# Optimization experiments

Measured on AMD Instinct MI355X. Metric: run time of the kernel, lower is better.

The kernel has to match this reference:

```python
import jax, jax.numpy as jnp
import numpy as np

B, IN_SIZE, P = 16384, 4096, 8
D = IN_SIZE // P  # 512


def setup_inputs() -> dict:
    key = jax.random.key(0)
    ks = jax.random.split(key, 10)
    bound = 1.0 / np.sqrt(D)  # fan_in = int_dim
    return {
        "x": jax.random.normal(ks[0], (B, IN_SIZE), dtype=jnp.float32),
        "weights1": jax.random.uniform(ks[1], (P, D, D), jnp.float32, -bound, bound),
        "bias1": jax.random.uniform(ks[2], (IN_SIZE,), jnp.float32, -bound, bound),
        "weights2": jax.random.uniform(ks[3], (P, D, D), jnp.float32, -bound, bound),
        "bias2": jax.random.uniform(ks[4], (IN_SIZE,), jnp.float32, -bound, bound),
        # trainable swish params (init 0 as in torch code)
        "gamma1": jnp.zeros((IN_SIZE,), jnp.float32),
        "beta1": jnp.zeros((IN_SIZE,), jnp.float32),
        "gamma3": jnp.zeros((IN_SIZE,), jnp.float32),
        "beta3": jnp.zeros((IN_SIZE,), jnp.float32),
        # Affine norms (scalar gain/bias)
        "gain1": jnp.ones((1,), jnp.float32),
        "nbias1": jnp.zeros((1,), jnp.float32),
        "gain3": jnp.ones((1,), jnp.float32),
        "nbias3": jnp.zeros((1,), jnp.float32),
    }


def _swish(x, gamma, beta):
    # f(x) = (gamma + sigmoid(beta*x) * (1-gamma)) * x
    return (gamma + jax.nn.sigmoid(beta * x) * (1.0 - gamma)) * x


def _block_matmul(x, w):
    # x: [B, IN_SIZE] -> [B, P, D]; block-diagonal matmul == batched per-partition GEMM
    xb = x.reshape(x.shape[0], P, D)
    return jnp.einsum("bpd,pde->bpe", xb, w).reshape(x.shape[0], IN_SIZE)


def reference(x, weights1, bias1, weights2, bias2, gamma1, beta1, gamma3, beta3,
              gain1, nbias1, gain3, nbias3):
    o1 = _swish(_block_matmul(x * gain1 + nbias1, weights1) + bias1, gamma1, beta1)
    o2 = _swish(_block_matmul(o1 * gain3 + nbias3, weights2) + bias2, gamma3, beta3) + x
    return o2
```

## Files before the change

kernel.cpp:

```cpp
#include <hip/hip_runtime.h>
#include <cstdint>
#include <cstddef>


#define B_ROWS 16384
#define IN_SZ  4096
#define P_PART 8
#define D_DIM  512

typedef unsigned short ushort_t;
typedef __attribute__((ext_vector_type(8))) short short8;
typedef __attribute__((ext_vector_type(4))) float f32x4;

__device__ inline unsigned short f2bf(float f) {
  union { float f; unsigned int u; } c; c.f = f;
  unsigned int u = c.u;
  return (unsigned short)((u + 0x7fffu + ((u >> 16) & 1u)) >> 16);
}

__device__ inline void gld_to_lds16(const void* g, void* l) {
  __builtin_amdgcn_global_load_lds((const __attribute__((address_space(1))) void*)g,
                                   (__attribute__((address_space(3))) void*)l,
                                   16, 0, 0);
}

__global__ __launch_bounds__(256) void wconv_kernel(const float* __restrict__ w1,
                                                    const float* __restrict__ w2,
                                                    ushort_t* __restrict__ wt1,
                                                    ushort_t* __restrict__ wt2) {
  __shared__ float tile[64][68];
  const int p = blockIdx.z & 7;
  const float*  src = (blockIdx.z < 8) ? w1 : w2;
  ushort_t*     dst = (blockIdx.z < 8) ? wt1 : wt2;
  const int k0 = blockIdx.x * 64;
  const int n0 = blockIdx.y * 64;
  const int t = threadIdx.x;

  const float* base = src + ((size_t)p * D_DIM + k0) * D_DIM + n0;
#pragma unroll
  for (int i = 0; i < 4; ++i) {
    int f = t + i * 256;
    int kr = f >> 4;
    int c4 = f & 15;
    float4 v = *(const float4*)(base + (size_t)kr * D_DIM + c4 * 4);
    *(float4*)(&tile[kr][c4 * 4]) = v;
  }
  __syncthreads();
  ushort_t* obase = dst + ((size_t)p * D_DIM + n0) * D_DIM + k0;
#pragma unroll
  for (int i = 0; i < 4; ++i) {
    int f = t + i * 256;
    int nr = f >> 4;
    int kc = (f & 15) * 4;
    unsigned int lo = f2bf(tile[kc + 0][nr]) | ((unsigned int)f2bf(tile[kc + 1][nr]) << 16);
    unsigned int hi = f2bf(tile[kc + 2][nr]) | ((unsigned int)f2bf(tile[kc + 3][nr]) << 16);
    uint2 pk; pk.x = lo; pk.y = hi;
    *(uint2*)(obase + (size_t)nr * D_DIM + kc) = pk;
  }
}

__global__ __launch_bounds__(256) void gemm1_kernel(
    const float* __restrict__ x, const ushort_t* __restrict__ wt1,
    const float* __restrict__ bias1, const float* __restrict__ gamma1,
    const float* __restrict__ beta1,
    const float* __restrict__ gain1, const float* __restrict__ nbias1,
    const float* __restrict__ gain3, const float* __restrict__ nbias3,
    ushort_t* __restrict__ o1) {
  __shared__ __align__(16) ushort_t As[128 * 64];
  __shared__ __align__(16) ushort_t Bs[128 * 64];

  const int t = threadIdx.x;
  const int lane = t & 63, wid = t >> 6;
  const int wm = wid & 1, wn = wid >> 1;
  const int l15 = lane & 15, quad = lane >> 4;
  const int m0 = blockIdx.x * 128;
  const int n0 = blockIdx.y * 128;
  const int p  = blockIdx.z;

  const float g1 = gain1[0], nb1 = nbias1[0];
  const float g3 = gain3[0], nb3 = nbias3[0];

  f32x4 acc[4][4];
#pragma unroll
  for (int i = 0; i < 4; ++i)
#pragma unroll
    for (int j = 0; j < 4; ++j) acc[i][j] = (f32x4)(0.0f);

  const ushort_t* wbase = wt1 + (size_t)p * D_DIM * D_DIM;

  for (int kt = 0; kt < 8; ++kt) {
    __syncthreads();
    const float* xtile = x + (size_t)m0 * IN_SZ + p * D_DIM + kt * 64;
#pragma unroll
    for (int i = 0; i < 8; ++i) {
      int f = t + i * 256;
      int row = f >> 4, c4 = f & 15;
      float4 v = *(const float4*)(xtile + (size_t)row * IN_SZ + c4 * 4);
      v.x = v.x * g1 + nb1; v.y = v.y * g1 + nb1;
      v.z = v.z * g1 + nb1; v.w = v.w * g1 + nb1;
      uint2 pk;
      pk.x = f2bf(v.x) | ((unsigned int)f2bf(v.y) << 16);
      pk.y = f2bf(v.z) | ((unsigned int)f2bf(v.w) << 16);
      *(uint2*)(&As[f * 4]) = pk;
    }
#pragma unroll
    for (int c = 0; c < 4; ++c) {
      int off = (wid * 4 + c) * 1024;
      int lb = off + lane * 16;
      int n = lb >> 7, kb = lb & 127;
      const ushort_t* g = wbase + (size_t)(n0 + n) * D_DIM + kt * 64 + (kb >> 1);
      gld_to_lds16(g, (char*)Bs + off);
    }
    __syncthreads();
#pragma unroll
    for (int kk = 0; kk < 2; ++kk) {
      const int kof = kk * 32 + quad * 8;
      short8 a[4], b[4];
#pragma unroll
      for (int i = 0; i < 4; ++i)
        a[i] = *(const short8*)(&As[(wm * 64 + i * 16 + l15) * 64 + kof]);
#pragma unroll
      for (int j = 0; j < 4; ++j)
        b[j] = *(const short8*)(&Bs[(wn * 64 + j * 16 + l15) * 64 + kof]);
#pragma unroll
      for (int i = 0; i < 4; ++i)
#pragma unroll
        for (int j = 0; j < 4; ++j)
          acc[i][j] = __builtin_amdgcn_mfma_f32_16x16x32_bf16(a[i], b[j], acc[i][j], 0, 0, 0);
    }
  }

  const int colg0 = p * D_DIM + n0 + wn * 64;
  const int row0 = m0 + wm * 64 + quad * 4;
#pragma unroll
  for (int j = 0; j < 4; ++j) {
    int col = colg0 + j * 16 + l15;
    float bv = bias1[col], ga = gamma1[col], be = beta1[col];
#pragma unroll
    for (int i = 0; i < 4; ++i) {
      int r0 = row0 + i * 16;
#pragma unroll
      for (int r = 0; r < 4; ++r) {
        float v = acc[i][j][r] + bv;
        float sg = 1.0f / (1.0f + __expf(-be * v));
        float o = (ga + sg * (1.0f - ga)) * v;
        o = o * g3 + nb3;
        o1[(size_t)(r0 + r) * IN_SZ + col] = f2bf(o);
      }
    }
  }
}

__global__ __launch_bounds__(256) void gemm2_kernel(
    const ushort_t* __restrict__ o1, const ushort_t* __restrict__ wt2,
    const float* __restrict__ bias2, const float* __restrict__ gamma3,
    const float* __restrict__ beta3,
    const float* __restrict__ x, float* __restrict__ out) {
  __shared__ __align__(16) ushort_t As[128 * 64];
  __shared__ __align__(16) ushort_t Bs[128 * 64];

  const int t = threadIdx.x;
  const int lane = t & 63, wid = t >> 6;
  const int wm = wid & 1, wn = wid >> 1;
  const int l15 = lane & 15, quad = lane >> 4;
  const int m0 = blockIdx.x * 128;
  const int n0 = blockIdx.y * 128;
  const int p  = blockIdx.z;

  f32x4 acc[4][4];
#pragma unroll
  for (int i = 0; i < 4; ++i)
#pragma unroll
    for (int j = 0; j < 4; ++j) acc[i][j] = (f32x4)(0.0f);

  const ushort_t* wbase = wt2 + (size_t)p * D_DIM * D_DIM;

  for (int kt = 0; kt < 8; ++kt) {
    __syncthreads();
#pragma unroll
    for (int c = 0; c < 4; ++c) {
      int off = (wid * 4 + c) * 1024;
      int lb = off + lane * 16;
      int m = lb >> 7, kb = lb & 127;
      const ushort_t* g = o1 + (size_t)(m0 + m) * IN_SZ + p * D_DIM + kt * 64 + (kb >> 1);
      gld_to_lds16(g, (char*)As + off);
    }
#pragma unroll
    for (int c = 0; c < 4; ++c) {
      int off = (wid * 4 + c) * 1024;
      int lb = off + lane * 16;
      int n = lb >> 7, kb = lb & 127;
      const ushort_t* g = wbase + (size_t)(n0 + n) * D_DIM + kt * 64 + (kb >> 1);
      gld_to_lds16(g, (char*)Bs + off);
    }
    __syncthreads();
#pragma unroll
    for (int kk = 0; kk < 2; ++kk) {
      const int kof = kk * 32 + quad * 8;
      short8 a[4], b[4];
#pragma unroll
      for (int i = 0; i < 4; ++i)
        a[i] = *(const short8*)(&As[(wm * 64 + i * 16 + l15) * 64 + kof]);
#pragma unroll
      for (int j = 0; j < 4; ++j)
        b[j] = *(const short8*)(&Bs[(wn * 64 + j * 16 + l15) * 64 + kof]);
#pragma unroll
      for (int i = 0; i < 4; ++i)
#pragma unroll
        for (int j = 0; j < 4; ++j)
          acc[i][j] = __builtin_amdgcn_mfma_f32_16x16x32_bf16(a[i], b[j], acc[i][j], 0, 0, 0);
    }
  }

  const int colg0 = p * D_DIM + n0 + wn * 64;
  const int row0 = m0 + wm * 64 + quad * 4;
#pragma unroll
  for (int j = 0; j < 4; ++j) {
    int col = colg0 + j * 16 + l15;
    float bv = bias2[col], ga = gamma3[col], be = beta3[col];
#pragma unroll
    for (int i = 0; i < 4; ++i) {
      int r0 = row0 + i * 16;
#pragma unroll
      for (int r = 0; r < 4; ++r) {
        float v = acc[i][j][r] + bv;
        float sg = 1.0f / (1.0f + __expf(-be * v));
        float o = (ga + sg * (1.0f - ga)) * v;
        size_t idx = (size_t)(r0 + r) * IN_SZ + col;
        out[idx] = o + x[idx];
      }
    }
  }
}

extern "C" void kernel_launch(void* const* d_in, const int* in_sizes, int n_in,
                              void* d_out, int out_size, void* d_ws, size_t ws_size,
                              hipStream_t stream) {
  const float* x      = (const float*)d_in[0];
  const float* w1     = (const float*)d_in[1];
  const float* b1     = (const float*)d_in[2];
  const float* w2     = (const float*)d_in[3];
  const float* b2     = (const float*)d_in[4];
  const float* gamma1 = (const float*)d_in[5];
  const float* beta1  = (const float*)d_in[6];
  const float* gamma3 = (const float*)d_in[7];
  const float* beta3  = (const float*)d_in[8];
  const float* gain1  = (const float*)d_in[9];
  const float* nbias1 = (const float*)d_in[10];
  const float* gain3  = (const float*)d_in[11];
  const float* nbias3 = (const float*)d_in[12];
  float* out = (float*)d_out;

  ushort_t* o1  = (ushort_t*)d_ws;
  ushort_t* wt1 = (ushort_t*)((char*)d_ws + (size_t)B_ROWS * IN_SZ * 2);
  ushort_t* wt2 = wt1 + (size_t)P_PART * D_DIM * D_DIM;

  wconv_kernel<<<dim3(8, 8, 16), 256, 0, stream>>>(w1, w2, wt1, wt2);
  gemm1_kernel<<<dim3(128, 4, 8), 256, 0, stream>>>(x, wt1, b1, gamma1, beta1,
                                                    gain1, nbias1, gain3, nbias3, o1);
  gemm2_kernel<<<dim3(128, 4, 8), 256, 0, stream>>>(o1, wt2, b2, gamma3, beta3, x, out);
}
```

Before: 866.6 us.

## Fuse both block GEMMs into one kernel keeping intermediate in swizzled LDS

Replaces the two separate GEMM kernels with one fused kernel. Each block owns a 64-row by 512-column slab of one partition, and the first layer's activation stays in XOR-swizzled shared memory instead of going through a global bf16 buffer. Weight fragments are now read straight from global memory (L2) by each wave instead of being staged in LDS. This removes the global write and re-read of the intermediate and one launch. The cost is 64KB of LDS per block, 128 accumulators per thread (occupancy pressure), and uncoalesced per-lane weight loads from global.

```diff
diff --git a/kernel.cpp b/kernel.cpp
--- a/kernel.cpp
+++ b/kernel.cpp
@@ -18,10 +18,9 @@
   return (unsigned short)((u + 0x7fffu + ((u >> 16) & 1u)) >> 16);
 }
 
-__device__ inline void gld_to_lds16(const void* g, void* l) {
-  __builtin_amdgcn_global_load_lds((const __attribute__((address_space(1))) void*)g,
-                                   (__attribute__((address_space(3))) void*)l,
-                                   16, 0, 0);
+__device__ inline int sw_off(int m, int k) {
+  int c = k >> 3;
+  return (m << 9) | (((c ^ (m & 7)) << 3) | (k & 7));
 }
 
 __global__ __launch_bounds__(256) void wconv_kernel(const float* __restrict__ w1,
@@ -59,174 +58,119 @@
   }
 }
 
-__global__ __launch_bounds__(256) void gemm1_kernel(
-    const float* __restrict__ x, const ushort_t* __restrict__ wt1,
+__device__ inline void gemm_k512(const ushort_t* __restrict__ xs,
+                                 const ushort_t* __restrict__ wp,
+                                 int l15, int quad, f32x4 acc[4][8]) {
+  for (int kk = 0; kk < 16; ++kk) {
+    const int k0 = kk * 32 + quad * 8;
+    short8 a[4];
+#pragma unroll
+    for (int i = 0; i < 4; ++i)
+      a[i] = *(const short8*)(&xs[sw_off(i * 16 + l15, k0)]);
+#pragma unroll
+    for (int jh = 0; jh < 2; ++jh) {
+      short8 b[4];
+#pragma unroll
+      for (int j = 0; j < 4; ++j)
+        b[j] = *(const short8*)(wp + (size_t)(jh * 64 + j * 16 + l15) * D_DIM + k0);
+#pragma unroll
+      for (int i = 0; i < 4; ++i)
+#pragma unroll
+        for (int j = 0; j < 4; ++j)
+          acc[i][jh * 4 + j] =
+              __builtin_amdgcn_mfma_f32_16x16x32_bf16(a[i], b[j], acc[i][jh * 4 + j], 0, 0, 0);
+    }
+  }
+}
+
+__global__ __launch_bounds__(256, 2) void fused_kernel(
+    const float* __restrict__ x,
+    const ushort_t* __restrict__ wt1, const ushort_t* __restrict__ wt2,
     const float* __restrict__ bias1, const float* __restrict__ gamma1,
     const float* __restrict__ beta1,
+    const float* __restrict__ bias2, const float* __restrict__ gamma3,
+    const float* __restrict__ beta3,
     const float* __restrict__ gain1, const float* __restrict__ nbias1,
     const float* __restrict__ gain3, const float* __restrict__ nbias3,
-    ushort_t* __restrict__ o1) {
-  __shared__ __align__(16) ushort_t As[128 * 64];
-  __shared__ __align__(16) ushort_t Bs[128 * 64];
+    float* __restrict__ out) {
+  __shared__ __align__(16) ushort_t xs[64 * 512];
 
   const int t = threadIdx.x;
-  const int lane = t & 63, wid = t >> 6;
-  const int wm = wid & 1, wn = wid >> 1;
+  const int lane = t & 63, w = t >> 6;
   const int l15 = lane & 15, quad = lane >> 4;
-  const int m0 = blockIdx.x * 128;
-  const int n0 = blockIdx.y * 128;
-  const int p  = blockIdx.z;
+  const int p = blockIdx.x;
+  const int m0 = blockIdx.y * 64;
 
   const float g1 = gain1[0], nb1 = nbias1[0];
   const float g3 = gain3[0], nb3 = nbias3[0];
 
-  f32x4 acc[4][4];
+  const float* xg = x + (size_t)m0 * IN_SZ + p * D_DIM;
+#pragma unroll
+  for (int i = 0; i < 32; ++i) {
+    int f = t + i * 256;
+    int row = f >> 7, c4 = f & 127;
+    float4 v = *(const float4*)(xg + (size_t)row * IN_SZ + c4 * 4);
+    v.x = v.x * g1 + nb1; v.y = v.y * g1 + nb1;
+    v.z = v.z * g1 + nb1; v.w = v.w * g1 + nb1;
+    uint2 pk;
+    pk.x = f2bf(v.x) | ((unsigned int)f2bf(v.y) << 16);
+    pk.y = f2bf(v.z) | ((unsigned int)f2bf(v.w) << 16);
+    *(uint2*)(&xs[sw_off(row, c4 * 4)]) = pk;
+  }
+  __syncthreads();
+
+  f32x4 acc[4][8];
 #pragma unroll
   for (int i = 0; i < 4; ++i)
 #pragma unroll
-    for (int j = 0; j < 4; ++j) acc[i][j] = (f32x4)(0.0f);
-
-  const ushort_t* wbase = wt1 + (size_t)p * D_DIM * D_DIM;
-
-  for (int kt = 0; kt < 8; ++kt) {
-    __syncthreads();
-    const float* xtile = x + (size_t)m0 * IN_SZ + p * D_DIM + kt * 64;
-#pragma unroll
-    for (int i = 0; i < 8; ++i) {
-      int f = t + i * 256;
-      int row = f >> 4, c4 = f & 15;
-      float4 v = *(const float4*)(xtile + (size_t)row * IN_SZ + c4 * 4);
-      v.x = v.x * g1 + nb1; v.y = v.y * g1 + nb1;
-      v.z = v.z * g1 + nb1; v.w = v.w * g1 + nb1;
-      uint2 pk;
-      pk.x = f2bf(v.x) | ((unsigned int)f2bf(v.y) << 16);
-      pk.y = f2bf(v.z) | ((unsigned int)f2bf(v.w) << 16);
-      *(uint2*)(&As[f * 4]) = pk;
-    }
-#pragma unroll
-    for (int c = 0; c < 4; ++c) {
-      int off = (wid * 4 + c) * 1024;
-      int lb = off + lane * 16;
-      int n = lb >> 7, kb = lb & 127;
-      const ushort_t* g = wbase + (size_t)(n0 + n) * D_DIM + kt * 64 + (kb >> 1);
-      gld_to_lds16(g, (char*)Bs + off);
-    }
-    __syncthreads();
-#pragma unroll
-    for (int kk = 0; kk < 2; ++kk) {
-      const int kof = kk * 32 + quad * 8;
-      short8 a[4], b[4];
-#pragma unroll
-      for (int i = 0; i < 4; ++i)
-        a[i] = *(const short8*)(&As[(wm * 64 + i * 16 + l15) * 64 + kof]);
-#pragma unroll
-      for (int j = 0; j < 4; ++j)
-        b[j] = *(const short8*)(&Bs[(wn * 64 + j * 16 + l15) * 64 + kof]);
-#pragma unroll
-      for (int i = 0; i < 4; ++i)
-#pragma unroll
-        for (int j = 0; j < 4; ++j)
-          acc[i][j] = __builtin_amdgcn_mfma_f32_16x16x32_bf16(a[i], b[j], acc[i][j], 0, 0, 0);
-    }
-  }
-
-  const int colg0 = p * D_DIM + n0 + wn * 64;
-  const int row0 = m0 + wm * 64 + quad * 4;
-#pragma unroll
-  for (int j = 0; j < 4; ++j) {
-    int col = colg0 + j * 16 + l15;
+    for (int j = 0; j < 8; ++j) acc[i][j] = (f32x4)(0.0f);
+
+  const ushort_t* w1p = wt1 + (size_t)p * D_DIM * D_DIM + (size_t)(w * 128) * D_DIM;
+  gemm_k512(xs, w1p, l15, quad, acc);
+
+  __syncthreads();
+
+#pragma unroll
+  for (int j = 0; j < 8; ++j) {
+    int nloc = w * 128 + j * 16 + l15;
+    int col = p * D_DIM + nloc;
     float bv = bias1[col], ga = gamma1[col], be = beta1[col];
 #pragma unroll
     for (int i = 0; i < 4; ++i) {
-      int r0 = row0 + i * 16;
 #pragma unroll
       for (int r = 0; r < 4; ++r) {
+        int m = i * 16 + quad * 4 + r;
         float v = acc[i][j][r] + bv;
         float sg = 1.0f / (1.0f + __expf(-be * v));
         float o = (ga + sg * (1.0f - ga)) * v;
         o = o * g3 + nb3;
-        o1[(size_t)(r0 + r) * IN_SZ + col] = f2bf(o);
+        xs[sw_off(m, nloc)] = f2bf(o);
       }
     }
   }
-}
-
-__global__ __launch_bounds__(256) void gemm2_kernel(
-    const ushort_t* __restrict__ o1, const ushort_t* __restrict__ wt2,
-    const float* __restrict__ bias2, const float* __restrict__ gamma3,
-    const float* __restrict__ beta3,
-    const float* __restrict__ x, float* __restrict__ out) {
-  __shared__ __align__(16) ushort_t As[128 * 64];
-  __shared__ __align__(16) ushort_t Bs[128 * 64];
-
-  const int t = threadIdx.x;
-  const int lane = t & 63, wid = t >> 6;
-  const int wm = wid & 1, wn = wid >> 1;
-  const int l15 = lane & 15, quad = lane >> 4;
-  const int m0 = blockIdx.x * 128;
-  const int n0 = blockIdx.y * 128;
-  const int p  = blockIdx.z;
-
-  f32x4 acc[4][4];
+  __syncthreads();
+
 #pragma unroll
   for (int i = 0; i < 4; ++i)
 #pragma unroll
-    for (int j = 0; j < 4; ++j) acc[i][j] = (f32x4)(0.0f);
-
-  const ushort_t* wbase = wt2 + (size_t)p * D_DIM * D_DIM;
-
-  for (int kt = 0; kt < 8; ++kt) {
-    __syncthreads();
-#pragma unroll
-    for (int c = 0; c < 4; ++c) {
-      int off = (wid * 4 + c) * 1024;
-      int lb = off + lane * 16;
-      int m = lb >> 7, kb = lb & 127;
-      const ushort_t* g = o1 + (size_t)(m0 + m) * IN_SZ + p * D_DIM + kt * 64 + (kb >> 1);
-      gld_to_lds16(g, (char*)As + off);
-    }
-#pragma unroll
-    for (int c = 0; c < 4; ++c) {
-      int off = (wid * 4 + c) * 1024;
-      int lb = off + lane * 16;
-      int n = lb >> 7, kb = lb & 127;
-      const ushort_t* g = wbase + (size_t)(n0 + n) * D_DIM + kt * 64 + (kb >> 1);
-      gld_to_lds16(g, (char*)Bs + off);
-    }
-    __syncthreads();
-#pragma unroll
-    for (int kk = 0; kk < 2; ++kk) {
-      const int kof = kk * 32 + quad * 8;
-      short8 a[4], b[4];
-#pragma unroll
-      for (int i = 0; i < 4; ++i)
-        a[i] = *(const short8*)(&As[(wm * 64 + i * 16 + l15) * 64 + kof]);
-#pragma unroll
-      for (int j = 0; j < 4; ++j)
-        b[j] = *(const short8*)(&Bs[(wn * 64 + j * 16 + l15) * 64 + kof]);
-#pragma unroll
-      for (int i = 0; i < 4; ++i)
-#pragma unroll
-        for (int j = 0; j < 4; ++j)
-          acc[i][j] = __builtin_amdgcn_mfma_f32_16x16x32_bf16(a[i], b[j], acc[i][j], 0, 0, 0);
-    }
-  }
-
-  const int colg0 = p * D_DIM + n0 + wn * 64;
-  const int row0 = m0 + wm * 64 + quad * 4;
-#pragma unroll
-  for (int j = 0; j < 4; ++j) {
-    int col = colg0 + j * 16 + l15;
+    for (int j = 0; j < 8; ++j) acc[i][j] = (f32x4)(0.0f);
+
+  const ushort_t* w2p = wt2 + (size_t)p * D_DIM * D_DIM + (size_t)(w * 128) * D_DIM;
+  gemm_k512(xs, w2p, l15, quad, acc);
+
+#pragma unroll
+  for (int j = 0; j < 8; ++j) {
+    int col = p * D_DIM + w * 128 + j * 16 + l15;
     float bv = bias2[col], ga = gamma3[col], be = beta3[col];
 #pragma unroll
     for (int i = 0; i < 4; ++i) {
-      int r0 = row0 + i * 16;
 #pragma unroll
       for (int r = 0; r < 4; ++r) {
+        int row = m0 + i * 16 + quad * 4 + r;
         float v = acc[i][j][r] + bv;
         float sg = 1.0f / (1.0f + __expf(-be * v));
         float o = (ga + sg * (1.0f - ga)) * v;
-        size_t idx = (size_t)(r0 + r) * IN_SZ + col;
+        size_t idx = (size_t)row * IN_SZ + col;
         out[idx] = o + x[idx];
       }
     }
@@ -251,12 +195,11 @@
   const float* nbias3 = (const float*)d_in[12];
   float* out = (float*)d_out;
 
-  ushort_t* o1  = (ushort_t*)d_ws;
-  ushort_t* wt1 = (ushort_t*)((char*)d_ws + (size_t)B_ROWS * IN_SZ * 2);
+  ushort_t* wt1 = (ushort_t*)d_ws;
   ushort_t* wt2 = wt1 + (size_t)P_PART * D_DIM * D_DIM;
 
   wconv_kernel<<<dim3(8, 8, 16), 256, 0, stream>>>(w1, w2, wt1, wt2);
-  gemm1_kernel<<<dim3(128, 4, 8), 256, 0, stream>>>(x, wt1, b1, gamma1, beta1,
-                                                    gain1, nbias1, gain3, nbias3, o1);
-  gemm2_kernel<<<dim3(128, 4, 8), 256, 0, stream>>>(o1, wt2, b2, gamma3, beta3, x, out);
-}
+  fused_kernel<<<dim3(P_PART, B_ROWS / 64), 256, 0, stream>>>(
+      x, wt1, wt2, b1, gamma1, beta1, b2, gamma3, beta3,
+      gain1, nbias1, gain3, nbias3, out);
+}
```

After: 875.9 us. No clear change (+1.1%).
